# Kernel tuning notes

Measured on AMD Instinct MI355X. Metric: run time of the kernel, lower is better.

The kernel has to match this reference:

```python
import jax, jax.numpy as jnp
import numpy as np

MU = 1.0  # opts.loss_type[1]


def setup_inputs() -> dict:
    key = jax.random.key(0)
    k1, k2 = jax.random.split(key)
    B, D, N = 8, 3, 4096
    srcs = jax.random.normal(k1, (B, D, N), dtype=jnp.float32)
    tgts = jax.random.normal(k2, (B, D, N), dtype=jnp.float32)
    return {"srcs": srcs, "tgts": tgts}


def reference(srcs, tgts):
    # [B, D, N] -> [B, N, D]
    s = jnp.transpose(srcs, (0, 2, 1))
    t = jnp.transpose(tgts, (0, 2, 1))
    # squared euclidean pairwise distances: ||s_i - t_j||^2, [B, N, M]
    s_sq = jnp.sum(s * s, axis=-1)          # [B, N]
    t_sq = jnp.sum(t * t, axis=-1)          # [B, M]
    cross = jnp.einsum('bnd,bmd->bnm', s, t)  # [B, N, M]
    P = s_sq[:, :, None] + t_sq[:, None, :] - 2.0 * cross
    # bidirectional chamfer mins
    d_tgt = jnp.min(P, axis=1)  # min over src points, [B, M]
    d_src = jnp.min(P, axis=2)  # min over tgt points, [B, N]
    distances = jnp.stack([d_tgt, d_src], axis=-1)  # [B, N, 2]
    # Geman-McClure robust penalty
    losses = (MU * distances / (distances + MU)).sum(axis=2).mean(axis=1).mean()
    return losses
```

## Files before the change

kernel.cpp:

```cpp
#include <hip/hip_runtime.h>


#define NPTS 4096
#define NB   8

typedef __attribute__((ext_vector_type(8)))  short bf16x8;
typedef __attribute__((ext_vector_type(16))) float floatx16;

#define OFF_APACK_S 0u
#define OFF_APACK_T (1u << 20)
#define OFF_BPACK_S (2u << 20)
#define OFF_BPACK_T (3u << 20)
#define OFF_BSUM    (4u << 20)

union V16 { int4 i; bf16x8 h; };

__device__ __forceinline__ unsigned short f2bf(float f) {
    unsigned u = __float_as_uint(f);
    u += 0x7FFFu + ((u >> 16) & 1u);
    return (unsigned short)(u >> 16);
}
__device__ __forceinline__ float bf2f(unsigned short h) {
    return __uint_as_float(((unsigned)h) << 16);
}
__device__ __forceinline__ int pk(unsigned short lo, unsigned short hi) {
    return (int)((unsigned)lo | ((unsigned)hi << 16));
}

__device__ __forceinline__ void pack_point(const float* __restrict__ cloud,
                                           int b, int j, int gid,
                                           char* __restrict__ apack,
                                           char* __restrict__ bpack) {
    const unsigned short ONE = 0x3F80;
    const float* p = cloud + b * 3 * NPTS;
    const float x = p[j], y = p[NPTS + j], z = p[2 * NPTS + j];
    const unsigned short hx = f2bf(x), hy = f2bf(y), hz = f2bf(z);
    const unsigned short lx = f2bf(x - bf2f(hx));
    const unsigned short ly = f2bf(y - bf2f(hy));
    const unsigned short lz = f2bf(z - bf2f(hz));
    const unsigned short a0 = f2bf(-2.0f * bf2f(hx));
    const unsigned short a1 = f2bf(-2.0f * bf2f(hy));
    const unsigned short a2 = f2bf(-2.0f * bf2f(hz));
    const unsigned short m0 = f2bf(-2.0f * (x - bf2f(hx)));
    const unsigned short m1 = f2bf(-2.0f * (y - bf2f(hy)));
    const unsigned short m2 = f2bf(-2.0f * (z - bf2f(hz)));
    const float n2 = fmaf(z, z, fmaf(y, y, x * x));
    const unsigned short n2h = f2bf(n2);
    const unsigned short n2l = f2bf(n2 - bf2f(n2h));

    int4* Ap = (int4*)(apack + (size_t)gid * 32);
    Ap[0] = make_int4(pk(a0, a1), pk(a2, m0), pk(m1, m2), pk(a0, a1));
    Ap[1] = make_int4(pk(a2, n2h), pk(n2l, ONE), pk(ONE, 0), 0);

    int4* Bp = (int4*)(bpack + (size_t)gid * 32);
    Bp[0] = make_int4(pk(hx, hy), pk(hz, hx), pk(hy, hz), pk(lx, ly));
    Bp[1] = make_int4(pk(lz, ONE), pk(ONE, n2h), pk(n2l, 0), 0);
}

__global__ __launch_bounds__(256)
void transform_kernel(const float* __restrict__ srcs,
                      const float* __restrict__ tgts,
                      char* __restrict__ ws) {
    const int gid = blockIdx.x * 256 + threadIdx.x;
    const int b = gid >> 12, j = gid & 4095;
    pack_point(srcs, b, j, gid, ws + OFF_APACK_S, ws + OFF_BPACK_S);
    pack_point(tgts, b, j, gid, ws + OFF_APACK_T, ws + OFF_BPACK_T);
}

__global__ __launch_bounds__(512, 4)
void chamfer_kernel(char* __restrict__ ws) {
    const int blk    = blockIdx.x;
    const int group  = blk & 15;
    const int dir    = group >> 3;
    const int b      = group & 7;
    const int stripe = blk >> 4;
    const int tid    = threadIdx.x;
    const int wave   = tid >> 6;
    const int lane   = tid & 63;
    const int l31    = lane & 31;
    const int half   = lane >> 5;

    const char* Ap = ws + (dir == 0 ? OFF_APACK_S : OFF_APACK_T);
    const char* Bp = ws + (dir == 0 ? OFF_BPACK_T : OFF_BPACK_S);

    V16 av0, av1;
    av0.i = *(const int4*)(Ap + (size_t)(b * NPTS + stripe * 64 + l31) * 32 + half * 16);
    av1.i = *(const int4*)(Ap + (size_t)(b * NPTS + stripe * 64 + 32 + l31) * 32 + half * 16);

    floatx16 rmin0, rmin1, zero;
#pragma unroll
    for (int r = 0; r < 16; r++) { rmin0[r] = 3.0e38f; rmin1[r] = 3.0e38f; zero[r] = 0.0f; }

    const int ct0 = wave * 16;
    const char* bbase = Bp + (size_t)(b * NPTS + ct0 * 32 + l31) * 32 + half * 16;

    V16 t0, t1, t2, t3;
    t0.i = *(const int4*)(bbase);
    t1.i = *(const int4*)(bbase + 1024);
    t2.i = *(const int4*)(bbase + 2048);
    t3.i = *(const int4*)(bbase + 3072);

#pragma unroll
    for (int i = 0; i < 16; i += 4) {
        V16 n0, n1, n2, n3;
        n0.i = *(const int4*)(bbase + (size_t)((i + 4) & 15) * 1024);
        n1.i = *(const int4*)(bbase + (size_t)((i + 5) & 15) * 1024);
        n2.i = *(const int4*)(bbase + (size_t)((i + 6) & 15) * 1024);
        n3.i = *(const int4*)(bbase + (size_t)((i + 7) & 15) * 1024);
#pragma unroll
        for (int u = 0; u < 4; u++) {
            const bf16x8 bf = (u == 0 ? t0.h : u == 1 ? t1.h : u == 2 ? t2.h : t3.h);
            const floatx16 d0 =
                __builtin_amdgcn_mfma_f32_32x32x16_bf16(av0.h, bf, zero, 0, 0, 0);
            const floatx16 d1 =
                __builtin_amdgcn_mfma_f32_32x32x16_bf16(av1.h, bf, zero, 0, 0, 0);
#pragma unroll
            for (int r = 0; r < 16; r++) {
                rmin0[r] = fminf(rmin0[r], d0[r]);
                rmin1[r] = fminf(rmin1[r], d1[r]);
            }
        }
        t0 = n0; t1 = n1; t2 = n2; t3 = n3;
    }

#pragma unroll
    for (int off = 1; off < 32; off <<= 1) {
#pragma unroll
        for (int r = 0; r < 16; r++) {
            rmin0[r] = fminf(rmin0[r], __shfl_xor(rmin0[r], off, 64));
            rmin1[r] = fminf(rmin1[r], __shfl_xor(rmin1[r], off, 64));
        }
    }
    __shared__ float sRow[8][64];
    if (l31 == 0) {
#pragma unroll
        for (int r = 0; r < 16; r++) {
            const int row = (r & 3) + 8 * (r >> 2) + 4 * half;
            sRow[wave][row]      = rmin0[r];
            sRow[wave][32 + row] = rmin1[r];
        }
    }
    __syncthreads();
    if (tid < 64) {
        float m = 3.0e38f;
#pragma unroll
        for (int w = 0; w < 8; w++) m = fminf(m, sRow[w][tid]);
        m = fmaxf(m, 0.0f);
        float g = m / (m + 1.0f);
#pragma unroll
        for (int off = 1; off < 64; off <<= 1)
            g += __shfl_xor(g, off, 64);
        if (tid == 0)
            ((float*)(ws + OFF_BSUM))[blk] = g;
    }
}

__global__ __launch_bounds__(256)
void finish_kernel(const char* __restrict__ ws, float* __restrict__ out) {
    const float* bsum = (const float*)(ws + OFF_BSUM);
    const int tid = threadIdx.x;
    float g = bsum[tid] + bsum[tid + 256] + bsum[tid + 512] + bsum[tid + 768];
#pragma unroll
    for (int off = 1; off < 64; off <<= 1)
        g += __shfl_xor(g, off, 64);
    __shared__ float sp[4];
    if ((tid & 63) == 0) sp[tid >> 6] = g;
    __syncthreads();
    if (tid == 0)
        out[0] = (sp[0] + sp[1] + sp[2] + sp[3]) * (1.0f / (NB * NPTS));
}

extern "C" void kernel_launch(void* const* d_in, const int* in_sizes, int n_in,
                              void* d_out, int out_size, void* d_ws, size_t ws_size,
                              hipStream_t stream) {
    const float* srcs = (const float*)d_in[0];
    const float* tgts = (const float*)d_in[1];
    float* out = (float*)d_out;
    char* ws = (char*)d_ws;

    transform_kernel<<<dim3(128), dim3(256), 0, stream>>>(srcs, tgts, ws);
    chamfer_kernel<<<dim3(1024), dim3(512), 0, stream>>>(ws);
    finish_kernel<<<dim3(1), dim3(256), 0, stream>>>(ws, out);
}
```

Measured before the change: 79.44 us.

## Switch chamfer tiles from 32x32x16 to 16x16x32 MFMA with duplicated K

Replaces the 32x32x16 bf16 MFMA with the 16x16x32 variant. Each stripe now covers 32 rows instead of 64 and each wave covers 32 target tiles of 16 columns, so the grid doubles to 2048 blocks and the final reduction reads 8 partial sums per thread. Because a packed point holds only 16 bf16 values, the two upper K quarters duplicate the lower ones, which doubles each distance; the result is halved before the robust penalty. This cuts accumulator registers per lane from 16 to 4, which may help occupancy and shorten reductions, but it doubles the matrix-core work per useful distance.

```diff
diff --git a/kernel.cpp b/kernel.cpp
--- a/kernel.cpp
+++ b/kernel.cpp
@@ -4,8 +4,8 @@
 #define NPTS 4096
 #define NB   8
 
-typedef __attribute__((ext_vector_type(8)))  short bf16x8;
-typedef __attribute__((ext_vector_type(16))) float floatx16;
+typedef __attribute__((ext_vector_type(8))) short bf16x8;
+typedef __attribute__((ext_vector_type(4))) float floatx4;
 
 #define OFF_APACK_S 0u
 #define OFF_APACK_T (1u << 20)
@@ -77,45 +77,45 @@
     const int tid    = threadIdx.x;
     const int wave   = tid >> 6;
     const int lane   = tid & 63;
-    const int l31    = lane & 31;
-    const int half   = lane >> 5;
+    const int l15    = lane & 15;
+    const int quad   = lane >> 4;
 
     const char* Ap = ws + (dir == 0 ? OFF_APACK_S : OFF_APACK_T);
     const char* Bp = ws + (dir == 0 ? OFF_BPACK_T : OFF_BPACK_S);
 
     V16 av0, av1;
-    av0.i = *(const int4*)(Ap + (size_t)(b * NPTS + stripe * 64 + l31) * 32 + half * 16);
-    av1.i = *(const int4*)(Ap + (size_t)(b * NPTS + stripe * 64 + 32 + l31) * 32 + half * 16);
+    av0.i = *(const int4*)(Ap + (size_t)(b * NPTS + stripe * 32 + l15) * 32 + (quad & 1) * 16);
+    av1.i = *(const int4*)(Ap + (size_t)(b * NPTS + stripe * 32 + 16 + l15) * 32 + (quad & 1) * 16);
 
-    floatx16 rmin0, rmin1, zero;
-#pragma unroll
-    for (int r = 0; r < 16; r++) { rmin0[r] = 3.0e38f; rmin1[r] = 3.0e38f; zero[r] = 0.0f; }
+    floatx4 rmin0 = {3.0e38f, 3.0e38f, 3.0e38f, 3.0e38f};
+    floatx4 rmin1 = rmin0;
+    const floatx4 zero = {0.0f, 0.0f, 0.0f, 0.0f};
 
-    const int ct0 = wave * 16;
-    const char* bbase = Bp + (size_t)(b * NPTS + ct0 * 32 + l31) * 32 + half * 16;
+    const int ct0 = wave * 32;
+    const char* bbase = Bp + (size_t)(b * NPTS + ct0 * 16 + l15) * 32 + (quad & 1) * 16;
 
     V16 t0, t1, t2, t3;
     t0.i = *(const int4*)(bbase);
-    t1.i = *(const int4*)(bbase + 1024);
-    t2.i = *(const int4*)(bbase + 2048);
-    t3.i = *(const int4*)(bbase + 3072);
+    t1.i = *(const int4*)(bbase + 512);
+    t2.i = *(const int4*)(bbase + 1024);
+    t3.i = *(const int4*)(bbase + 1536);
 
 #pragma unroll
-    for (int i = 0; i < 16; i += 4) {
+    for (int i = 0; i < 32; i += 4) {
         V16 n0, n1, n2, n3;
-        n0.i = *(const int4*)(bbase + (size_t)((i + 4) & 15) * 1024);
-        n1.i = *(const int4*)(bbase + (size_t)((i + 5) & 15) * 1024);
-        n2.i = *(const int4*)(bbase + (size_t)((i + 6) & 15) * 1024);
-        n3.i = *(const int4*)(bbase + (size_t)((i + 7) & 15) * 1024);
+        n0.i = *(const int4*)(bbase + (size_t)((i + 4) & 31) * 512);
+        n1.i = *(const int4*)(bbase + (size_t)((i + 5) & 31) * 512);
+        n2.i = *(const int4*)(bbase + (size_t)((i + 6) & 31) * 512);
+        n3.i = *(const int4*)(bbase + (size_t)((i + 7) & 31) * 512);
 #pragma unroll
         for (int u = 0; u < 4; u++) {
             const bf16x8 bf = (u == 0 ? t0.h : u == 1 ? t1.h : u == 2 ? t2.h : t3.h);
-            const floatx16 d0 =
-                __builtin_amdgcn_mfma_f32_32x32x16_bf16(av0.h, bf, zero, 0, 0, 0);
-            const floatx16 d1 =
-                __builtin_amdgcn_mfma_f32_32x32x16_bf16(av1.h, bf, zero, 0, 0, 0);
+            const floatx4 d0 =
+                __builtin_amdgcn_mfma_f32_16x16x32_bf16(av0.h, bf, zero, 0, 0, 0);
+            const floatx4 d1 =
+                __builtin_amdgcn_mfma_f32_16x16x32_bf16(av1.h, bf, zero, 0, 0, 0);
 #pragma unroll
-            for (int r = 0; r < 16; r++) {
+            for (int r = 0; r < 4; r++) {
                 rmin0[r] = fminf(rmin0[r], d0[r]);
                 rmin1[r] = fminf(rmin1[r], d1[r]);
             }
@@ -124,31 +124,30 @@
     }
 
 #pragma unroll
-    for (int off = 1; off < 32; off <<= 1) {
+    for (int off = 1; off < 16; off <<= 1) {
 #pragma unroll
-        for (int r = 0; r < 16; r++) {
+        for (int r = 0; r < 4; r++) {
             rmin0[r] = fminf(rmin0[r], __shfl_xor(rmin0[r], off, 64));
             rmin1[r] = fminf(rmin1[r], __shfl_xor(rmin1[r], off, 64));
         }
     }
-    __shared__ float sRow[8][64];
-    if (l31 == 0) {
+    __shared__ float sRow[8][32];
+    if (l15 == 0) {
 #pragma unroll
-        for (int r = 0; r < 16; r++) {
-            const int row = (r & 3) + 8 * (r >> 2) + 4 * half;
-            sRow[wave][row]      = rmin0[r];
-            sRow[wave][32 + row] = rmin1[r];
+        for (int r = 0; r < 4; r++) {
+            sRow[wave][quad * 4 + r]      = rmin0[r];
+            sRow[wave][16 + quad * 4 + r] = rmin1[r];
         }
     }
     __syncthreads();
-    if (tid < 64) {
+    if (tid < 32) {
         float m = 3.0e38f;
 #pragma unroll
         for (int w = 0; w < 8; w++) m = fminf(m, sRow[w][tid]);
-        m = fmaxf(m, 0.0f);
+        m = fmaxf(m * 0.5f, 0.0f);
         float g = m / (m + 1.0f);
 #pragma unroll
-        for (int off = 1; off < 64; off <<= 1)
+        for (int off = 1; off < 32; off <<= 1)
             g += __shfl_xor(g, off, 64);
         if (tid == 0)
             ((float*)(ws + OFF_BSUM))[blk] = g;
@@ -159,7 +158,9 @@
 void finish_kernel(const char* __restrict__ ws, float* __restrict__ out) {
     const float* bsum = (const float*)(ws + OFF_BSUM);
     const int tid = threadIdx.x;
-    float g = bsum[tid] + bsum[tid + 256] + bsum[tid + 512] + bsum[tid + 768];
+    float g = 0.0f;
+#pragma unroll
+    for (int k = 0; k < 8; k++) g += bsum[tid + k * 256];
 #pragma unroll
     for (int off = 1; off < 64; off <<= 1)
         g += __shfl_xor(g, off, 64);
@@ -179,6 +180,6 @@
     char* ws = (char*)d_ws;
 
     transform_kernel<<<dim3(128), dim3(256), 0, stream>>>(srcs, tgts, ws);
-    chamfer_kernel<<<dim3(1024), dim3(512), 0, stream>>>(ws);
+    chamfer_kernel<<<dim3(2048), dim3(512), 0, stream>>>(ws);
     finish_kernel<<<dim3(1), dim3(256), 0, stream>>>(ws, out);
 }
```

Result: faster. 77.25 us (-2.8%).
